# Kernel optimization log

Hardware: AMD Instinct MI355X
Metric: run time of the kernel (lower is better)

The kernel has to match this reference:

```python
import jax, jax.numpy as jnp
import numpy as np

N = 50000
E = 800000
IN_DIM = 128
HID = 128


def setup_inputs() -> dict:
    key = jax.random.key(0)
    ks = jax.random.split(key, 8)
    x = jax.random.normal(ks[0], (N, IN_DIM), dtype=jnp.float32)
    edge_index = jax.random.randint(ks[1], (2, E), 0, N, dtype=jnp.int64)
    s1 = 1.0 / np.sqrt(IN_DIM)
    s2 = 1.0 / np.sqrt(HID)
    Wl1 = jax.random.uniform(ks[2], (HID, IN_DIM), jnp.float32, -s1, s1)
    bl1 = jnp.zeros((HID,), jnp.float32)
    Wr1 = jax.random.uniform(ks[3], (HID, IN_DIM), jnp.float32, -s1, s1)
    Wl2 = jax.random.uniform(ks[4], (HID, HID), jnp.float32, -s2, s2)
    bl2 = jnp.zeros((HID,), jnp.float32)
    Wr2 = jax.random.uniform(ks[5], (HID, HID), jnp.float32, -s2, s2)
    return {"x": x, "Wl1": Wl1, "bl1": bl1, "Wr1": Wr1,
            "Wl2": Wl2, "bl2": bl2, "Wr2": Wr2, "edge_index": edge_index}


def _sage_layer(h, src, dst, deg_inv, Wl, bl, Wr):
    # mean aggregation over in-edges: gather source feats, scatter-sum to targets
    msg_sum = jax.ops.segment_sum(h[src], dst, num_segments=N)  # [N, d]
    agg = msg_sum * deg_inv[:, None]
    return agg @ Wl.T + bl + h @ Wr.T


def reference(x, Wl1, bl1, Wr1, Wl2, bl2, Wr2, edge_index):
    src, dst = edge_index[0], edge_index[1]
    deg = jax.ops.segment_sum(jnp.ones((E,), x.dtype), dst, num_segments=N)
    deg_inv = 1.0 / jnp.maximum(deg, 1.0)
    h = jax.nn.relu(_sage_layer(x, src, dst, deg_inv, Wl1, bl1, Wr1))
    h = jax.nn.relu(_sage_layer(h, src, dst, deg_inv, Wl2, bl2, Wr2))
    return h  # dropout is identity in eval mode
```

## Files before the change

### kernel.cpp

```cpp
#include <hip/hip_runtime.h>

#define N_NODES 50000
#define N_ROWS_PAD 50064
#define N_EDGES 800000
#define DIM 128
#define KCAT 256
#define CAP 64
#define MPITCH 264

#define PACK_N (2 * DIM * KCAT)
#define CAST_N (N_NODES * 16)
#define PREP_TOTAL (PACK_N + CAST_N + N_EDGES)

typedef unsigned int u32;
typedef unsigned short u16;
typedef __attribute__((ext_vector_type(8))) short short8;
typedef __attribute__((ext_vector_type(4))) float f32x4;

static __device__ __forceinline__ u16 f2bf(float f) {
  union { float f; u32 u; } v; v.f = f;
  u32 r = v.u + 0x7fffu + ((v.u >> 16) & 1u);
  return (u16)(r >> 16);
}
static __device__ __forceinline__ float bflo(u32 p) { return __uint_as_float(p << 16); }
static __device__ __forceinline__ float bfhi(u32 p) { return __uint_as_float(p & 0xffff0000u); }

__global__ void prep(const float* __restrict__ wl1, const float* __restrict__ wr1,
                     const float* __restrict__ wl2, const float* __restrict__ wr2,
                     const float* __restrict__ x,
                     const int* __restrict__ src, const int* __restrict__ dst,
                     int* __restrict__ cnt, u16* __restrict__ csr,
                     u16* __restrict__ wcat, u32* __restrict__ bufx) {
  int idx = blockIdx.x * blockDim.x + threadIdx.x;
  if (idx < PACK_N) {
    int layer = idx >> 15;
    int n = (idx >> 8) & 127;
    int k = idx & 255;
    const float* wl = layer ? wl2 : wl1;
    const float* wr = layer ? wr2 : wr1;
    float v = (k < DIM) ? wl[n * DIM + k] : wr[n * DIM + (k - DIM)];
    wcat[idx] = f2bf(v);
  } else if (idx < PACK_N + CAST_N) {
    int t = idx - PACK_N;
    int node = t >> 4, q = t & 15;
    float4 v0 = ((const float4*)x)[(size_t)node * 32 + q * 2];
    float4 v1 = ((const float4*)x)[(size_t)node * 32 + q * 2 + 1];
    uint4 p;
    p.x = (u32)f2bf(v0.x) | ((u32)f2bf(v0.y) << 16);
    p.y = (u32)f2bf(v0.z) | ((u32)f2bf(v0.w) << 16);
    p.z = (u32)f2bf(v1.x) | ((u32)f2bf(v1.y) << 16);
    p.w = (u32)f2bf(v1.z) | ((u32)f2bf(v1.w) << 16);
    ((uint4*)bufx)[(size_t)node * 16 + q] = p;
  } else {
    int e = idx - (PACK_N + CAST_N);
    if (e < N_EDGES) {
      int d = dst[e];
      int pos = atomicAdd(&cnt[d], 1);
      if (pos < CAP)
        __builtin_nontemporal_store((u16)src[e], &csr[(size_t)pos * N_NODES + d]);
    }
  }
}

__global__ __launch_bounds__(256) void fused_layer(
    const u16* __restrict__ hin, const u16* __restrict__ csr,
    const int* __restrict__ cnt, const u16* __restrict__ wcat,
    const float* __restrict__ bias, float* __restrict__ fout,
    u16* __restrict__ bout) {
  __shared__ u16 smsg[16 * MPITCH];
  const int lane = threadIdx.x & 63;
  const int wv = threadIdx.x >> 6;
  const int row0 = blockIdx.x * 16;
  const int sub = lane >> 4, q = lane & 15;
  const uint4* h16 = (const uint4*)hin;

  for (int r = 0; r < 4; ++r) {
    int node = row0 + wv * 4 + r;
    if (node >= N_NODES) break;
    int craw = cnt[node];
    int c = min(craw, CAP);
    const u16* col = csr + node;
    float a0 = 0, a1 = 0, a2 = 0, a3 = 0, a4 = 0, a5 = 0, a6 = 0, a7 = 0;
#define ACC8(u) { a0 += bflo(u.x); a1 += bfhi(u.x); a2 += bflo(u.y); a3 += bfhi(u.y); \
                  a4 += bflo(u.z); a5 += bfhi(u.z); a6 += bflo(u.w); a7 += bfhi(u.w); }
    int i = sub;
    for (; i + 12 < c; i += 16) {
      u32 s0 = col[(size_t)i * N_NODES];
      u32 s1 = col[(size_t)(i + 4) * N_NODES];
      u32 s2 = col[(size_t)(i + 8) * N_NODES];
      u32 s3 = col[(size_t)(i + 12) * N_NODES];
      uint4 u0 = h16[(size_t)s0 * 16 + q];
      uint4 u1 = h16[(size_t)s1 * 16 + q];
      uint4 u2 = h16[(size_t)s2 * 16 + q];
      uint4 u3 = h16[(size_t)s3 * 16 + q];
      ACC8(u0); ACC8(u1); ACC8(u2); ACC8(u3);
    }
    for (; i < c; i += 4) {
      uint4 u0 = h16[(size_t)((u32)col[(size_t)i * N_NODES]) * 16 + q];
      ACC8(u0);
    }
#undef ACC8
    a0 += __shfl_xor(a0, 16); a1 += __shfl_xor(a1, 16);
    a2 += __shfl_xor(a2, 16); a3 += __shfl_xor(a3, 16);
    a4 += __shfl_xor(a4, 16); a5 += __shfl_xor(a5, 16);
    a6 += __shfl_xor(a6, 16); a7 += __shfl_xor(a7, 16);
    a0 += __shfl_xor(a0, 32); a1 += __shfl_xor(a1, 32);
    a2 += __shfl_xor(a2, 32); a3 += __shfl_xor(a3, 32);
    a4 += __shfl_xor(a4, 32); a5 += __shfl_xor(a5, 32);
    a6 += __shfl_xor(a6, 32); a7 += __shfl_xor(a7, 32);
    if (lane < 16) {
      float di = 1.0f / (float)max(craw, 1);
      uint4 p;
      p.x = (u32)f2bf(a0 * di) | ((u32)f2bf(a1 * di) << 16);
      p.y = (u32)f2bf(a2 * di) | ((u32)f2bf(a3 * di) << 16);
      p.z = (u32)f2bf(a4 * di) | ((u32)f2bf(a5 * di) << 16);
      p.w = (u32)f2bf(a6 * di) | ((u32)f2bf(a7 * di) << 16);
      *(uint4*)&smsg[(wv * 4 + r) * MPITCH + q * 8] = p;
    }
  }
  __syncthreads();

  const int l15 = lane & 15;
  const int ch = lane >> 4;
  const short8* bp = (const short8*)(wcat + (size_t)l15 * KCAT + ch * 8);

  f32x4 acc[2];
  acc[0] = (f32x4){0.f, 0.f, 0.f, 0.f};
  acc[1] = (f32x4){0.f, 0.f, 0.f, 0.f};

#pragma unroll
  for (int ks = 0; ks < 4; ++ks) {
    short8 a = *(const short8*)&smsg[l15 * MPITCH + ch * 8 + ks * 32];
#pragma unroll
    for (int t = 0; t < 2; ++t) {
      int nt = wv * 2 + t;
      acc[t] = __builtin_amdgcn_mfma_f32_16x16x32_bf16(a, bp[nt * 512 + ks * 4],
                                                       acc[t], 0, 0, 0);
    }
  }
  const short8* ap = (const short8*)(hin + (size_t)(row0 + l15) * DIM + ch * 8);
#pragma unroll
  for (int ks = 0; ks < 4; ++ks) {
    short8 a = ap[ks * 4];
#pragma unroll
    for (int t = 0; t < 2; ++t) {
      int nt = wv * 2 + t;
      acc[t] = __builtin_amdgcn_mfma_f32_16x16x32_bf16(
          a, bp[nt * 512 + (4 + ks) * 4], acc[t], 0, 0, 0);
    }
  }

  const int rbase = row0 + (ch << 2);
#pragma unroll
  for (int t = 0; t < 2; ++t) {
    int colj = (wv * 2 + t) * 16 + l15;
    float bb = bias[colj];
#pragma unroll
    for (int r = 0; r < 4; ++r) {
      int row = rbase + r;
      if (row < N_NODES) {
        float v = fmaxf(acc[t][r] + bb, 0.f);
        if (fout) fout[(size_t)row * DIM + colj] = v;
        if (bout) bout[(size_t)row * DIM + colj] = f2bf(v);
      }
    }
  }
}

extern "C" void kernel_launch(void* const* d_in, const int* in_sizes, int n_in,
                              void* d_out, int out_size, void* d_ws, size_t ws_size,
                              hipStream_t stream) {
  const float* x   = (const float*)d_in[0];
  const float* Wl1 = (const float*)d_in[1];
  const float* bl1 = (const float*)d_in[2];
  const float* Wr1 = (const float*)d_in[3];
  const float* Wl2 = (const float*)d_in[4];
  const float* bl2 = (const float*)d_in[5];
  const float* Wr2 = (const float*)d_in[6];
  const int* eidx  = (const int*)d_in[7];
  const int* src = eidx;
  const int* dst = eidx + N_EDGES;
  float* out = (float*)d_out;

  char* ws = (char*)d_ws;
  int* cnt  = (int*)ws;
  u16* csr  = (u16*)(ws + 256 * 1024);
  u16* wcat = (u16*)(ws + 6815744);
  u16* bufx = (u16*)(ws + 6946816);
  u16* bufh = (u16*)(ws + 19763200);

  hipMemsetAsync(cnt, 0, N_NODES * sizeof(int), stream);

  prep<<<PREP_TOTAL / 256, 256, 0, stream>>>(Wl1, Wr1, Wl2, Wr2, x, src, dst,
                                             cnt, csr, wcat, (u32*)bufx);

  const int grid = N_ROWS_PAD / 16;

  fused_layer<<<grid, 256, 0, stream>>>(bufx, csr, cnt, wcat, bl1,
                                        (float*)nullptr, bufh);
  fused_layer<<<grid, 256, 0, stream>>>(bufh, csr, cnt, wcat + DIM * KCAT, bl2,
                                        out, (u16*)nullptr);
}
```

Measured before the change: 278.8 us.

## Fuse memset, prep and both layers into one cooperative persistent kernel

Merges the count reset, the prep work (weight packing, input cast, CSR build) and both SAGE layers into one cooperative kernel that uses grid-wide syncs instead of separate launches. Blocks loop persistently over 16-row groups, with the grid sized from occupancy and capped at 1536. The intent is to remove launch gaps and the memset call. In exchange it adds grid-sync cost, limits parallelism to the resident blocks, and forces occupancy via launch bounds. The CSR store is no longer nontemporal, and a fallback path with separate kernels is kept.

```diff
diff --git a/kernel.cpp b/kernel.cpp
--- a/kernel.cpp
+++ b/kernel.cpp
@@ -1,12 +1,15 @@
 #include <hip/hip_runtime.h>
+#include <hip/hip_cooperative_groups.h>
+
+namespace cg = cooperative_groups;
 
 #define N_NODES 50000
-#define N_ROWS_PAD 50064
 #define N_EDGES 800000
 #define DIM 128
 #define KCAT 256
 #define CAP 64
 #define MPITCH 264
+#define NGROUPS 3125
 
 #define PACK_N (2 * DIM * KCAT)
 #define CAST_N (N_NODES * 16)
@@ -25,13 +28,12 @@
 static __device__ __forceinline__ float bflo(u32 p) { return __uint_as_float(p << 16); }
 static __device__ __forceinline__ float bfhi(u32 p) { return __uint_as_float(p & 0xffff0000u); }
 
-__global__ void prep(const float* __restrict__ wl1, const float* __restrict__ wr1,
-                     const float* __restrict__ wl2, const float* __restrict__ wr2,
-                     const float* __restrict__ x,
-                     const int* __restrict__ src, const int* __restrict__ dst,
-                     int* __restrict__ cnt, u16* __restrict__ csr,
-                     u16* __restrict__ wcat, u32* __restrict__ bufx) {
-  int idx = blockIdx.x * blockDim.x + threadIdx.x;
+static __device__ __forceinline__ void prep_item(
+    int idx, const float* __restrict__ wl1, const float* __restrict__ wr1,
+    const float* __restrict__ wl2, const float* __restrict__ wr2,
+    const float* __restrict__ x, const int* __restrict__ src,
+    const int* __restrict__ dst, int* __restrict__ cnt, u16* __restrict__ csr,
+    u16* __restrict__ wcat, u32* __restrict__ bufx) {
   if (idx < PACK_N) {
     int layer = idx >> 15;
     int n = (idx >> 8) & 127;
@@ -53,30 +55,25 @@
     ((uint4*)bufx)[(size_t)node * 16 + q] = p;
   } else {
     int e = idx - (PACK_N + CAST_N);
-    if (e < N_EDGES) {
-      int d = dst[e];
-      int pos = atomicAdd(&cnt[d], 1);
-      if (pos < CAP)
-        __builtin_nontemporal_store((u16)src[e], &csr[(size_t)pos * N_NODES + d]);
-    }
-  }
-}
-
-__global__ __launch_bounds__(256) void fused_layer(
-    const u16* __restrict__ hin, const u16* __restrict__ csr,
-    const int* __restrict__ cnt, const u16* __restrict__ wcat,
+    int d = dst[e];
+    int pos = atomicAdd(&cnt[d], 1);
+    if (pos < CAP) csr[(size_t)pos * N_NODES + d] = (u16)src[e];
+  }
+}
+
+static __device__ __forceinline__ void layer_group(
+    int rg, const u16* __restrict__ hin, const u16* __restrict__ csr,
+    const int* __restrict__ cnt, const u16* __restrict__ wcat_l,
     const float* __restrict__ bias, float* __restrict__ fout,
-    u16* __restrict__ bout) {
-  __shared__ u16 smsg[16 * MPITCH];
+    u16* __restrict__ bout, u16* smsg) {
   const int lane = threadIdx.x & 63;
   const int wv = threadIdx.x >> 6;
-  const int row0 = blockIdx.x * 16;
   const int sub = lane >> 4, q = lane & 15;
   const uint4* h16 = (const uint4*)hin;
+  const int row0 = rg * 16;
 
   for (int r = 0; r < 4; ++r) {
     int node = row0 + wv * 4 + r;
-    if (node >= N_NODES) break;
     int craw = cnt[node];
     int c = min(craw, CAP);
     const u16* col = csr + node;
@@ -122,12 +119,10 @@
 
   const int l15 = lane & 15;
   const int ch = lane >> 4;
-  const short8* bp = (const short8*)(wcat + (size_t)l15 * KCAT + ch * 8);
-
+  const short8* bp = (const short8*)(wcat_l + (size_t)l15 * KCAT + ch * 8);
   f32x4 acc[2];
   acc[0] = (f32x4){0.f, 0.f, 0.f, 0.f};
   acc[1] = (f32x4){0.f, 0.f, 0.f, 0.f};
-
 #pragma unroll
   for (int ks = 0; ks < 4; ++ks) {
     short8 a = *(const short8*)&smsg[l15 * MPITCH + ch * 8 + ks * 32];
@@ -149,7 +144,6 @@
           a, bp[nt * 512 + (4 + ks) * 4], acc[t], 0, 0, 0);
     }
   }
-
   const int rbase = row0 + (ch << 2);
 #pragma unroll
   for (int t = 0; t < 2; ++t) {
@@ -158,13 +152,67 @@
 #pragma unroll
     for (int r = 0; r < 4; ++r) {
       int row = rbase + r;
-      if (row < N_NODES) {
-        float v = fmaxf(acc[t][r] + bb, 0.f);
-        if (fout) fout[(size_t)row * DIM + colj] = v;
-        if (bout) bout[(size_t)row * DIM + colj] = f2bf(v);
-      }
-    }
-  }
+      float v = fmaxf(acc[t][r] + bb, 0.f);
+      if (fout) fout[(size_t)row * DIM + colj] = v;
+      if (bout) bout[(size_t)row * DIM + colj] = f2bf(v);
+    }
+  }
+}
+
+__global__ __launch_bounds__(256, 6) void mega(
+    const float* __restrict__ x,
+    const float* __restrict__ wl1, const float* __restrict__ wr1,
+    const float* __restrict__ wl2, const float* __restrict__ wr2,
+    const float* __restrict__ bl1, const float* __restrict__ bl2,
+    const int* __restrict__ src, const int* __restrict__ dst,
+    int* __restrict__ cnt, u16* __restrict__ csr, u16* __restrict__ wcat,
+    u16* __restrict__ bufx, u16* __restrict__ bufh, float* __restrict__ out) {
+  __shared__ u16 smsg[16 * MPITCH];
+  cg::grid_group grid = cg::this_grid();
+  const int nthr = gridDim.x * 256;
+  const int tid = blockIdx.x * 256 + threadIdx.x;
+
+  for (int i = tid; i < N_NODES; i += nthr) cnt[i] = 0;
+  __threadfence();
+  grid.sync();
+
+  for (int idx = tid; idx < PREP_TOTAL; idx += nthr)
+    prep_item(idx, wl1, wr1, wl2, wr2, x, src, dst, cnt, csr, wcat, (u32*)bufx);
+  __threadfence();
+  grid.sync();
+
+  for (int rg = blockIdx.x; rg < NGROUPS; rg += gridDim.x) {
+    layer_group(rg, bufx, csr, cnt, wcat, bl1, (float*)nullptr, bufh, smsg);
+    __syncthreads();
+  }
+  __threadfence();
+  grid.sync();
+
+  for (int rg = blockIdx.x; rg < NGROUPS; rg += gridDim.x) {
+    layer_group(rg, bufh, csr, cnt, wcat + DIM * KCAT, bl2, out, (u16*)nullptr,
+                smsg);
+    __syncthreads();
+  }
+}
+
+__global__ void prep_k(const float* __restrict__ wl1, const float* __restrict__ wr1,
+                       const float* __restrict__ wl2, const float* __restrict__ wr2,
+                       const float* __restrict__ x, const int* __restrict__ src,
+                       const int* __restrict__ dst, int* __restrict__ cnt,
+                       u16* __restrict__ csr, u16* __restrict__ wcat,
+                       u32* __restrict__ bufx) {
+  int idx = blockIdx.x * blockDim.x + threadIdx.x;
+  if (idx < PREP_TOTAL)
+    prep_item(idx, wl1, wr1, wl2, wr2, x, src, dst, cnt, csr, wcat, bufx);
+}
+
+__global__ __launch_bounds__(256) void fused_k(
+    const u16* __restrict__ hin, const u16* __restrict__ csr,
+    const int* __restrict__ cnt, const u16* __restrict__ wcat_l,
+    const float* __restrict__ bias, float* __restrict__ fout,
+    u16* __restrict__ bout) {
+  __shared__ u16 smsg[16 * MPITCH];
+  layer_group(blockIdx.x, hin, csr, cnt, wcat_l, bias, fout, bout, smsg);
 }
 
 extern "C" void kernel_launch(void* const* d_in, const int* in_sizes, int n_in,
@@ -189,15 +237,33 @@
   u16* bufx = (u16*)(ws + 6946816);
   u16* bufh = (u16*)(ws + 19763200);
 
-  hipMemsetAsync(cnt, 0, N_NODES * sizeof(int), stream);
-
-  prep<<<PREP_TOTAL / 256, 256, 0, stream>>>(Wl1, Wr1, Wl2, Wr2, x, src, dst,
-                                             cnt, csr, wcat, (u32*)bufx);
-
-  const int grid = N_ROWS_PAD / 16;
-
-  fused_layer<<<grid, 256, 0, stream>>>(bufx, csr, cnt, wcat, bl1,
-                                        (float*)nullptr, bufh);
-  fused_layer<<<grid, 256, 0, stream>>>(bufh, csr, cnt, wcat + DIM * KCAT, bl2,
-                                        out, (u16*)nullptr);
-}
+  int dev = 0, cus = 0, nblk = 0;
+  (void)hipGetDevice(&dev);
+  (void)hipDeviceGetAttribute(&cus, hipDeviceAttributeMultiprocessorCount, dev);
+  hipError_t oe = hipOccupancyMaxActiveBlocksPerMultiprocessor(&nblk, mega, 256, 0);
+  long g = (oe == hipSuccess && cus > 0) ? (long)nblk * cus : 0;
+  if (g > 1536) g = 1536;
+
+  bool done = false;
+  if (g >= 256) {
+    void* args[] = {
+        (void*)&x, (void*)&Wl1, (void*)&Wr1, (void*)&Wl2, (void*)&Wr2,
+        (void*)&bl1, (void*)&bl2, (void*)&src, (void*)&dst,
+        (void*)&cnt, (void*)&csr, (void*)&wcat, (void*)&bufx, (void*)&bufh,
+        (void*)&out};
+    hipError_t err = hipLaunchCooperativeKernel((void*)mega, dim3((int)g),
+                                                dim3(256), args, 0, stream);
+    if (err == hipSuccess) done = true;
+    else (void)hipGetLastError();
+  }
+
+  if (!done) {
+    (void)hipMemsetAsync(cnt, 0, N_NODES * sizeof(int), stream);
+    prep_k<<<(PREP_TOTAL + 255) / 256, 256, 0, stream>>>(
+        Wl1, Wr1, Wl2, Wr2, x, src, dst, cnt, csr, wcat, (u32*)bufx);
+    fused_k<<<NGROUPS, 256, 0, stream>>>(bufx, csr, cnt, wcat, bl1,
+                                         (float*)nullptr, bufh);
+    fused_k<<<NGROUPS, 256, 0, stream>>>(bufh, csr, cnt, wcat + DIM * KCAT, bl2,
+                                         out, (u16*)nullptr);
+  }
+}
```

New measurement: 750.5 us. +169.2%, slower.
